# Optimization experiments

Hardware: AMD Instinct MI355X
Metric: run time of the kernel (lower is better)

The kernel has to match this reference:

```python
import jax, jax.numpy as jnp
import numpy as np

B, D = 65536, 154

def setup_inputs() -> dict:
    key = jax.random.key(0)
    k1, k2, k3, k4, k5, k6 = jax.random.split(key, 6)
    recon_l = jax.random.normal(k1, (B, D), dtype=jnp.float32)
    recon_r = jax.random.normal(k2, (B, D), dtype=jnp.float32)
    KLD_l = jax.random.normal(k3, (B, D), dtype=jnp.float32)
    KLD_r = jax.random.normal(k4, (B, D), dtype=jnp.float32)
    lr = jax.random.randint(k5, (B,), 0, 3, dtype=jnp.int64)
    # f_pose in {-1, 0}: -1 marks invalid samples
    f_pose = jax.random.randint(k6, (B,), 0, 2, dtype=jnp.int64) - 1
    return {"recon_l": recon_l, "recon_r": recon_r, "KLD_l": KLD_l,
            "KLD_r": KLD_r, "lr": lr, "f_pose": f_pose}

def reference(recon_l, recon_r, KLD_l, KLD_r, lr, f_pose):
    valid = (f_pose != -1)
    use_l = (valid & ((lr == 0) | (lr == 2))).astype(recon_l.dtype)  # [B]
    use_r = (valid & ((lr == 1) | (lr == 2))).astype(recon_r.dtype)  # [B]
    # per-sample sums over 154-dim pose params, then masked batch reduction
    recon_loss_all = jnp.dot(use_l, recon_l.sum(axis=1)) + jnp.dot(use_r, recon_r.sum(axis=1))
    KLD_loss_all = jnp.dot(use_l, KLD_l.sum(axis=1)) + jnp.dot(use_r, KLD_r.sum(axis=1))
    count = (use_l.sum() + use_r.sum()).astype(jnp.int32)
    return (recon_loss_all / 154.0, KLD_loss_all, count)
```

## Files before the change

kernel.cpp:

```cpp
#include <hip/hip_runtime.h>


#define BB 65536
#define DD 154
#define N4 (BB * DD / 4)
#define BLOCKS 9856
#define THREADS 256

typedef float nt_float4 __attribute__((ext_vector_type(4)));

__global__ void zero_out_kernel(float* __restrict__ out) {
    if (threadIdx.x < 3) out[threadIdx.x] = 0.0f;
}

__device__ __forceinline__ float2 wpair(int l, int f) {
    const bool valid = (f != -1);
    float2 w;
    w.x = (valid && ((l == 0) || (l == 2))) ? 1.0f : 0.0f;
    w.y = (valid && ((l == 1) || (l == 2))) ? 1.0f : 0.0f;
    return w;
}

__global__ __launch_bounds__(THREADS) void pose_partial_kernel(
    const float* __restrict__ recon_l, const float* __restrict__ recon_r,
    const float* __restrict__ kld_l,   const float* __restrict__ kld_r,
    const int* __restrict__ lr,        const int* __restrict__ fp,
    float* __restrict__ ws,            float* __restrict__ out)
{
    const nt_float4* __restrict__ rl4 = (const nt_float4*)recon_l;
    const nt_float4* __restrict__ rr4 = (const nt_float4*)recon_r;
    const nt_float4* __restrict__ kl4 = (const nt_float4*)kld_l;
    const nt_float4* __restrict__ kr4 = (const nt_float4*)kld_r;

    const int i = blockIdx.x * THREADS + threadIdx.x;
    const int h = 2 * i;
    const int r0 = h / 77;
    const int r1 = (h + 1) / 77;

    const nt_float4 a = __builtin_nontemporal_load(&rl4[i]);
    const nt_float4 b = __builtin_nontemporal_load(&rr4[i]);
    const nt_float4 c = __builtin_nontemporal_load(&kl4[i]);
    const nt_float4 d = __builtin_nontemporal_load(&kr4[i]);

    const float2 w0 = wpair(lr[r0], fp[r0]);
    const float2 w1 = wpair(lr[r1], fp[r1]);

    float acc_recon = w0.x * (a.x + a.y) + w1.x * (a.z + a.w)
                    + w0.y * (b.x + b.y) + w1.y * (b.z + b.w);
    float acc_kld   = w0.x * (c.x + c.y) + w1.x * (c.z + c.w)
                    + w0.y * (d.x + d.y) + w1.y * (d.z + d.w);
    float acc_cnt = 0.0f;
    if (i < BB) {
        const float2 w = wpair(lr[i], fp[i]);
        acc_cnt = w.x + w.y;
    }

#pragma unroll
    for (int off = 32; off > 0; off >>= 1) {
        acc_recon += __shfl_down(acc_recon, off, 64);
        acc_kld   += __shfl_down(acc_kld,   off, 64);
        acc_cnt   += __shfl_down(acc_cnt,   off, 64);
    }

    __shared__ float s_recon[4], s_kld[4], s_cnt[4];
    const int wave = threadIdx.x >> 6;
    const int lane = threadIdx.x & 63;
    if (lane == 0) {
        s_recon[wave] = acc_recon;
        s_kld[wave]   = acc_kld;
        s_cnt[wave]   = acc_cnt;
    }
    __syncthreads();

    if (threadIdx.x == 0) {
        const float r = s_recon[0] + s_recon[1] + s_recon[2] + s_recon[3];
        const float k = s_kld[0]   + s_kld[1]   + s_kld[2]   + s_kld[3];
        const float n = s_cnt[0]   + s_cnt[1]   + s_cnt[2]   + s_cnt[3];
        if (ws != nullptr) {
            ws[blockIdx.x]              = r;
            ws[BLOCKS + blockIdx.x]     = k;
            ws[2 * BLOCKS + blockIdx.x] = n;
        } else {
            atomicAdd(&out[0], r * (1.0f / 154.0f));
            atomicAdd(&out[1], k);
            atomicAdd(&out[2], n);
        }
    }
}

__global__ __launch_bounds__(1024) void final_reduce_kernel(
    const float* __restrict__ ws, float* __restrict__ out)
{
    float r = 0.0f, k = 0.0f, n = 0.0f;
    for (int i = threadIdx.x; i < BLOCKS; i += 1024) {
        r += ws[i];
        k += ws[BLOCKS + i];
        n += ws[2 * BLOCKS + i];
    }
#pragma unroll
    for (int off = 32; off > 0; off >>= 1) {
        r += __shfl_down(r, off, 64);
        k += __shfl_down(k, off, 64);
        n += __shfl_down(n, off, 64);
    }
    __shared__ float s_r[16], s_k[16], s_n[16];
    const int wave = threadIdx.x >> 6;
    const int lane = threadIdx.x & 63;
    if (lane == 0) { s_r[wave] = r; s_k[wave] = k; s_n[wave] = n; }
    __syncthreads();
    if (threadIdx.x == 0) {
        float rr = 0.0f, kk = 0.0f, nn = 0.0f;
#pragma unroll
        for (int w = 0; w < 16; ++w) { rr += s_r[w]; kk += s_k[w]; nn += s_n[w]; }
        out[0] = rr * (1.0f / 154.0f);
        out[1] = kk;
        out[2] = nn;
    }
}

extern "C" void kernel_launch(void* const* d_in, const int* in_sizes, int n_in,
                              void* d_out, int out_size, void* d_ws, size_t ws_size,
                              hipStream_t stream) {
    const float* recon_l = (const float*)d_in[0];
    const float* recon_r = (const float*)d_in[1];
    const float* kld_l   = (const float*)d_in[2];
    const float* kld_r   = (const float*)d_in[3];
    const int*   lr      = (const int*)d_in[4];
    const int*   fp      = (const int*)d_in[5];
    float* out = (float*)d_out;

    const bool use_ws = (d_ws != nullptr) &&
                        (ws_size >= (size_t)(3 * BLOCKS) * sizeof(float));
    float* ws = use_ws ? (float*)d_ws : nullptr;

    if (!use_ws) {
        zero_out_kernel<<<1, 64, 0, stream>>>(out);
    }
    pose_partial_kernel<<<BLOCKS, THREADS, 0, stream>>>(
        recon_l, recon_r, kld_l, kld_r, lr, fp, ws, out);
    if (use_ws) {
        final_reduce_kernel<<<1, 1024, 0, stream>>>(ws, out);
    }
}
```

Measured before the change: 165.1 us.

## Fuse final reduction into partial kernel via last-block atomic counter

Replaces the separate final reduction kernel with a last-block-done pattern: each block writes its partial, fences, and bumps an atomic counter, and the last block reduces all partials. A small init kernel resets the counter, so the launch count stays the same. The count reduction now uses wave ballot plus popcount instead of shuffles, and is limited to the first BB/256 blocks. This targets the dependent tail kernel launch and some shuffle work, at the cost of a global atomic and fence per block.

```diff
diff --git a/kernel.cpp b/kernel.cpp
--- a/kernel.cpp
+++ b/kernel.cpp
@@ -6,8 +6,13 @@
 #define N4 (BB * DD / 4)
 #define BLOCKS 9856
 #define THREADS 256
+#define CNT_BLOCKS (BB / THREADS)
 
 typedef float nt_float4 __attribute__((ext_vector_type(4)));
+
+__global__ void init_ws_kernel(unsigned int* __restrict__ counter) {
+    if (threadIdx.x == 0) *counter = 0u;
+}
 
 __global__ void zero_out_kernel(float* __restrict__ out) {
     if (threadIdx.x < 3) out[threadIdx.x] = 0.0f;
@@ -25,7 +30,8 @@
     const float* __restrict__ recon_l, const float* __restrict__ recon_r,
     const float* __restrict__ kld_l,   const float* __restrict__ kld_r,
     const int* __restrict__ lr,        const int* __restrict__ fp,
-    float* __restrict__ ws,            float* __restrict__ out)
+    float* __restrict__ ws,            unsigned int* __restrict__ counter,
+    float* __restrict__ out)
 {
     const nt_float4* __restrict__ rl4 = (const nt_float4*)recon_l;
     const nt_float4* __restrict__ rr4 = (const nt_float4*)recon_r;
@@ -49,72 +55,72 @@
                     + w0.y * (b.x + b.y) + w1.y * (b.z + b.w);
     float acc_kld   = w0.x * (c.x + c.y) + w1.x * (c.z + c.w)
                     + w0.y * (d.x + d.y) + w1.y * (d.z + d.w);
-    float acc_cnt = 0.0f;
-    if (i < BB) {
+
+    float n_wave = 0.0f;
+    if (blockIdx.x < CNT_BLOCKS) {
         const float2 w = wpair(lr[i], fp[i]);
-        acc_cnt = w.x + w.y;
+        n_wave = (float)(__popcll(__ballot(w.x != 0.0f)) +
+                         __popcll(__ballot(w.y != 0.0f)));
     }
 
 #pragma unroll
     for (int off = 32; off > 0; off >>= 1) {
         acc_recon += __shfl_down(acc_recon, off, 64);
         acc_kld   += __shfl_down(acc_kld,   off, 64);
-        acc_cnt   += __shfl_down(acc_cnt,   off, 64);
     }
 
-    __shared__ float s_recon[4], s_kld[4], s_cnt[4];
+    __shared__ float s_r[4], s_k[4], s_n[4];
+    __shared__ int s_last;
     const int wave = threadIdx.x >> 6;
     const int lane = threadIdx.x & 63;
     if (lane == 0) {
-        s_recon[wave] = acc_recon;
-        s_kld[wave]   = acc_kld;
-        s_cnt[wave]   = acc_cnt;
+        s_r[wave] = acc_recon;
+        s_k[wave] = acc_kld;
+        s_n[wave] = n_wave;
     }
     __syncthreads();
 
-    if (threadIdx.x == 0) {
-        const float r = s_recon[0] + s_recon[1] + s_recon[2] + s_recon[3];
-        const float k = s_kld[0]   + s_kld[1]   + s_kld[2]   + s_kld[3];
-        const float n = s_cnt[0]   + s_cnt[1]   + s_cnt[2]   + s_cnt[3];
-        if (ws != nullptr) {
-            ws[blockIdx.x]              = r;
-            ws[BLOCKS + blockIdx.x]     = k;
-            ws[2 * BLOCKS + blockIdx.x] = n;
-        } else {
-            atomicAdd(&out[0], r * (1.0f / 154.0f));
-            atomicAdd(&out[1], k);
-            atomicAdd(&out[2], n);
+    if (ws != nullptr) {
+        if (threadIdx.x == 0) {
+            ws[blockIdx.x]              = s_r[0] + s_r[1] + s_r[2] + s_r[3];
+            ws[BLOCKS + blockIdx.x]     = s_k[0] + s_k[1] + s_k[2] + s_k[3];
+            ws[2 * BLOCKS + blockIdx.x] = s_n[0] + s_n[1] + s_n[2] + s_n[3];
+            __threadfence();
+            const unsigned int t = atomicAdd(counter, 1u);
+            s_last = (t == BLOCKS - 1u);
         }
-    }
-}
-
-__global__ __launch_bounds__(1024) void final_reduce_kernel(
-    const float* __restrict__ ws, float* __restrict__ out)
-{
-    float r = 0.0f, k = 0.0f, n = 0.0f;
-    for (int i = threadIdx.x; i < BLOCKS; i += 1024) {
-        r += ws[i];
-        k += ws[BLOCKS + i];
-        n += ws[2 * BLOCKS + i];
-    }
+        __syncthreads();
+        if (s_last) {
+            __threadfence();
+            const float4* __restrict__ p0 = (const float4*)ws;
+            const float4* __restrict__ p1 = (const float4*)(ws + BLOCKS);
+            const float4* __restrict__ p2 = (const float4*)(ws + 2 * BLOCKS);
+            float r = 0.0f, k = 0.0f, n = 0.0f;
+            for (int j = threadIdx.x; j < BLOCKS / 4; j += THREADS) {
+                const float4 v0 = p0[j]; r += v0.x + v0.y + v0.z + v0.w;
+                const float4 v1 = p1[j]; k += v1.x + v1.y + v1.z + v1.w;
+                const float4 v2 = p2[j]; n += v2.x + v2.y + v2.z + v2.w;
+            }
 #pragma unroll
-    for (int off = 32; off > 0; off >>= 1) {
-        r += __shfl_down(r, off, 64);
-        k += __shfl_down(k, off, 64);
-        n += __shfl_down(n, off, 64);
-    }
-    __shared__ float s_r[16], s_k[16], s_n[16];
-    const int wave = threadIdx.x >> 6;
-    const int lane = threadIdx.x & 63;
-    if (lane == 0) { s_r[wave] = r; s_k[wave] = k; s_n[wave] = n; }
-    __syncthreads();
-    if (threadIdx.x == 0) {
-        float rr = 0.0f, kk = 0.0f, nn = 0.0f;
-#pragma unroll
-        for (int w = 0; w < 16; ++w) { rr += s_r[w]; kk += s_k[w]; nn += s_n[w]; }
-        out[0] = rr * (1.0f / 154.0f);
-        out[1] = kk;
-        out[2] = nn;
+            for (int off = 32; off > 0; off >>= 1) {
+                r += __shfl_down(r, off, 64);
+                k += __shfl_down(k, off, 64);
+                n += __shfl_down(n, off, 64);
+            }
+            if (lane == 0) { s_r[wave] = r; s_k[wave] = k; s_n[wave] = n; }
+            __syncthreads();
+            if (threadIdx.x == 0) {
+                out[0] = (s_r[0] + s_r[1] + s_r[2] + s_r[3]) * (1.0f / 154.0f);
+                out[1] =  s_k[0] + s_k[1] + s_k[2] + s_k[3];
+                out[2] =  s_n[0] + s_n[1] + s_n[2] + s_n[3];
+            }
+        }
+    } else {
+        if (threadIdx.x == 0) {
+            atomicAdd(&out[0], (s_r[0] + s_r[1] + s_r[2] + s_r[3]) * (1.0f / 154.0f));
+            atomicAdd(&out[1],  s_k[0] + s_k[1] + s_k[2] + s_k[3]);
+            atomicAdd(&out[2],  s_n[0] + s_n[1] + s_n[2] + s_n[3]);
+        }
     }
 }
 
@@ -130,15 +136,16 @@
     float* out = (float*)d_out;
 
     const bool use_ws = (d_ws != nullptr) &&
-                        (ws_size >= (size_t)(3 * BLOCKS) * sizeof(float));
+                        (ws_size >= (size_t)(3 * BLOCKS + 1) * sizeof(float));
     float* ws = use_ws ? (float*)d_ws : nullptr;
+    unsigned int* counter = use_ws ? (unsigned int*)((float*)d_ws + 3 * BLOCKS)
+                                   : nullptr;
 
-    if (!use_ws) {
+    if (use_ws) {
+        init_ws_kernel<<<1, 64, 0, stream>>>(counter);
+    } else {
         zero_out_kernel<<<1, 64, 0, stream>>>(out);
     }
     pose_partial_kernel<<<BLOCKS, THREADS, 0, stream>>>(
-        recon_l, recon_r, kld_l, kld_r, lr, fp, ws, out);
-    if (use_ws) {
-        final_reduce_kernel<<<1, 1024, 0, stream>>>(ws, out);
-    }
+        recon_l, recon_r, kld_l, kld_r, lr, fp, ws, counter, out);
 }
```

After: 601.6 us. 3.64x slower.
